# Kernel tuning notes

Measured on AMD Instinct MI355X. Metric: run time of the kernel, lower is better.

## Reference

```python
import jax, jax.numpy as jnp
import numpy as np

EPS = 1e-5

def layernorm(x, gamma, beta):
    mu = jnp.mean(x, axis=-1, keepdims=True)
    var = jnp.var(x, axis=-1, keepdims=True)
    return (x - mu) * jax.lax.rsqrt(var + EPS) * gamma + beta

def setup_inputs() -> dict:
    key = jax.random.key(0)
    ks = jax.random.split(key, 8)
    B, N, D, H, Dh, M = 2, 2048, 768, 12, 64, 3072
    s = 0.02
    return {
        "x": jax.random.normal(ks[0], (B, N, D), jnp.float32),
        "Wqkv": jax.random.normal(ks[1], (D, 3 * H * Dh), jnp.float32) * s,
        "Wout": jax.random.normal(ks[2], (H * Dh, D), jnp.float32) * s,
        "gamma1": jnp.ones((D,), jnp.float32),
        "beta1": jnp.zeros((D,), jnp.float32),
        "gamma2": jnp.ones((D,), jnp.float32),
        "beta2": jnp.zeros((D,), jnp.float32),
        "W1": jax.random.normal(ks[3], (D, M), jnp.float32) * s,
        "b1": jnp.zeros((M,), jnp.float32),
        "W2": jax.random.normal(ks[4], (M, D), jnp.float32) * s,
        "b2": jnp.zeros((D,), jnp.float32),
        "attn_bias": jax.random.normal(ks[5], (1, H, N, N), jnp.float32) * 0.1,
    }

def reference(x, Wqkv, Wout, gamma1, beta1, gamma2, beta2, W1, b1, W2, b2, attn_bias):
    B, N, D = x.shape
    H = attn_bias.shape[1]
    Dh = Wqkv.shape[1] // (3 * H)
    scale = Dh ** -0.5
    # Attention block (pre-norm)
    h = layernorm(x, gamma1, beta1)
    qkv = h @ Wqkv                              # [B, N, 3*H*Dh]
    qkv = qkv.reshape(B, N, 3, H, Dh)
    q, k, v = (jnp.transpose(qkv[:, :, i], (0, 2, 1, 3)) for i in range(3))  # [B, H, N, Dh]
    dots = jnp.einsum('bhqd,bhkd->bhqk', q, k) * scale
    # pos_info == 'mul_att_normed'
    attn = jax.nn.softmax(dots, axis=-1) * jax.nn.softmax(attn_bias, axis=-1)
    attn = attn / jnp.sum(attn, axis=-1, keepdims=True)
    out = jnp.einsum('bhqk,bhkd->bhqd', attn, v)          # [B, H, N, Dh]
    out = jnp.transpose(out, (0, 2, 1, 3)).reshape(B, N, H * Dh)
    x = out @ Wout + x
    # FeedForward block (pre-norm)
    h = layernorm(x, gamma2, beta2)
    h = jax.nn.gelu(h @ W1 + b1, approximate=False)
    x = h @ W2 + b2 + x
    return x
```

## Files before the change

### kernel.cpp

```cpp
#include <hip/hip_runtime.h>

typedef unsigned short u16t;
typedef __bf16 bf16x8 __attribute__((ext_vector_type(8)));
typedef float  f32x4  __attribute__((ext_vector_type(4)));
typedef float  f32x16 __attribute__((ext_vector_type(16)));
typedef unsigned u32x2 __attribute__((ext_vector_type(2)));
typedef unsigned u32x4 __attribute__((ext_vector_type(4)));

#define DEV __device__ __forceinline__

DEV u16t f32_to_bf16(float f) {
    unsigned u = __float_as_uint(f);
    unsigned r = (u + 0x7FFFu + ((u >> 16) & 1u)) >> 16;
    return (u16t)r;
}
DEV float bf16_to_f32(u16t u) { return __uint_as_float((unsigned)u << 16); }

DEV unsigned cvt_pk_bf16(float lo, float hi) {
    unsigned r;
    asm("v_cvt_pk_bf16_f32 %0, %1, %2" : "=v"(r) : "v"(lo), "v"(hi));
    return r;
}

DEV float gelu_exact(float x) {
    return 0.5f * x * (1.0f + erff(x * 0.70710678118654752f));
}

DEV void glds16(const void* g, void* l) {
    __builtin_amdgcn_global_load_lds(
        (const __attribute__((address_space(1))) void*)g,
        (__attribute__((address_space(3))) void*)l, 16, 0, 0);
}

#define SCHED_FENCE() __builtin_amdgcn_sched_barrier(0)

#define WAITN_BARRIER(N)                                          \
    asm volatile("s_waitcnt vmcnt(" #N ")" ::: "memory");         \
    SCHED_FENCE();                                                \
    __builtin_amdgcn_s_barrier();                                 \
    SCHED_FENCE();

#define PLAIN_BARRIER()                                           \
    SCHED_FENCE();                                                \
    __builtin_amdgcn_s_barrier();                                 \
    SCHED_FENCE();

__global__ __launch_bounds__(192)
void ln_kernel(const float* __restrict__ x, const float* __restrict__ g,
               const float* __restrict__ b, u16t* __restrict__ out)
{
    const int row = blockIdx.x;
    const int t = threadIdx.x;
    const f32x4 v = *reinterpret_cast<const f32x4*>(x + (size_t)row * 768 + t * 4);
    float s  = v[0] + v[1] + v[2] + v[3];
    float s2 = v[0] * v[0] + v[1] * v[1] + v[2] * v[2] + v[3] * v[3];
#pragma unroll
    for (int off = 32; off > 0; off >>= 1) {
        s  += __shfl_xor(s, off);
        s2 += __shfl_xor(s2, off);
    }
    __shared__ float sm[6];
    const int w = t >> 6;
    if ((t & 63) == 0) { sm[w] = s; sm[3 + w] = s2; }
    __syncthreads();
    s  = sm[0] + sm[1] + sm[2];
    s2 = sm[3] + sm[4] + sm[5];
    const float mu  = s * (1.0f / 768.0f);
    const float var = fmaxf(s2 * (1.0f / 768.0f) - mu * mu, 0.0f);
    const float rst = rsqrtf(var + 1e-5f);
    const f32x4 gv = *reinterpret_cast<const f32x4*>(g + t * 4);
    const f32x4 bv = *reinterpret_cast<const f32x4*>(b + t * 4);
    u32x2 r;
    r[0] = cvt_pk_bf16((v[0] - mu) * rst * gv[0] + bv[0],
                       (v[1] - mu) * rst * gv[1] + bv[1]);
    r[1] = cvt_pk_bf16((v[2] - mu) * rst * gv[2] + bv[2],
                       (v[3] - mu) * rst * gv[3] + bv[3]);
    *reinterpret_cast<u32x2*>(out + (size_t)row * 768 + t * 4) = r;
}

__global__ __launch_bounds__(256)
void transpose_all(const float* __restrict__ Wqkv, const float* __restrict__ Wout,
                   const float* __restrict__ W1, const float* __restrict__ W2,
                   u16t* __restrict__ WqkvT, u16t* __restrict__ WoutT,
                   u16t* __restrict__ W1T, u16t* __restrict__ W2T)
{
    int b = blockIdx.x;
    const float* in; u16t* out; int R, C, cx, ry;
    if (b < 432)       { in = Wqkv; out = WqkvT; R = 768;  C = 2304; cx = b % 36; ry = b / 36; }
    else if (b < 576)  { b -= 432;  in = Wout; out = WoutT; R = 768;  C = 768;  cx = b % 12; ry = b / 12; }
    else if (b < 1152) { b -= 576;  in = W1;   out = W1T;   R = 768;  C = 3072; cx = b % 48; ry = b / 48; }
    else               { b -= 1152; in = W2;   out = W2T;   R = 3072; C = 768;  cx = b % 12; ry = b / 12; }
    __shared__ float tile[64][65];
    const int c0 = cx * 64, r0 = ry * 64;
    const int t = threadIdx.x;
#pragma unroll
    for (int j = 0; j < 16; ++j) {
        const int idx = j * 256 + t;
        const int rl = idx >> 6, cl = idx & 63;
        tile[rl][cl] = in[(size_t)(r0 + rl) * C + c0 + cl];
    }
    __syncthreads();
#pragma unroll
    for (int j = 0; j < 16; ++j) {
        const int idx = j * 256 + t;
        const int cl = idx >> 6, rl = idx & 63;
        out[(size_t)(c0 + cl) * R + r0 + rl] = f32_to_bf16(tile[rl][cl]);
    }
}

template <int MODE, int TM>
__global__ __launch_bounds__(256)
void gemm_kernel(const u16t* __restrict__ A, const u16t* __restrict__ BT,
                 float* __restrict__ Cf, u16t* __restrict__ Cb,
                 const float* __restrict__ bias, const float* __restrict__ res,
                 u16t* __restrict__ Qo, u16t* __restrict__ Ko,
                 u16t* __restrict__ VTo,
                 int M, int Nn, int K)
{
    constexpr int MI = TM / 32;
    constexpr int ABYTES = TM * 128;
    __shared__ __align__(16) char gsm[ABYTES + 16384];
    const int t = threadIdx.x;
    const int w = t >> 6, lane = t & 63;
    const int l16 = lane & 15, lhi = lane >> 4;
    const int wr = w >> 1, wc = w & 1;
    const int m0 = blockIdx.x * TM, n0 = blockIdx.y * 128;

    const f32x4 fz = {0.f, 0.f, 0.f, 0.f};
    f32x4 acc[MI][4];
#pragma unroll
    for (int i = 0; i < MI; ++i)
#pragma unroll
        for (int j = 0; j < 4; ++j) acc[i][j] = fz;

    const int rbase = t >> 3;
    const int ssrc = ((t & 7) ^ (rbase & 7)) * 16;

    auto stage = [&](int kt) {
#pragma unroll
        for (int i = 0; i < TM / 32; ++i) {
            const int row = i * 32 + rbase;
            glds16((const char*)A + ((size_t)(m0 + row) * K + kt) * 2 + ssrc,
                   gsm + i * 4096 + t * 16);
        }
#pragma unroll
        for (int i = 0; i < 4; ++i) {
            const int row = i * 32 + rbase;
            glds16((const char*)BT + ((size_t)(n0 + row) * K + kt) * 2 + ssrc,
                   gsm + ABYTES + i * 4096 + t * 16);
        }
    };

    auto body = [&]() {
        const char* Ab = gsm;
        const char* Bb = gsm + ABYTES;
#pragma unroll
        for (int ks = 0; ks < 2; ++ks) {
            const int wsl = lhi + 4 * ks;
            bf16x8 af[MI], bfv[4];
#pragma unroll
            for (int i = 0; i < MI; ++i) {
                const int row = 16 * MI * wr + 16 * i + l16;
                af[i] = *reinterpret_cast<const bf16x8*>(
                    Ab + row * 128 + ((wsl ^ (row & 7)) << 4));
            }
#pragma unroll
            for (int j = 0; j < 4; ++j) {
                const int row = 64 * wc + 16 * j + l16;
                bfv[j] = *reinterpret_cast<const bf16x8*>(
                    Bb + row * 128 + ((wsl ^ (row & 7)) << 4));
            }
#pragma unroll
            for (int i = 0; i < MI; ++i)
#pragma unroll
                for (int j = 0; j < 4; ++j)
                    acc[i][j] = __builtin_amdgcn_mfma_f32_16x16x32_bf16(
                        af[i], bfv[j], acc[i][j], 0, 0, 0);
        }
    };

    for (int kt = 0; kt < K; kt += 64) {
        stage(kt);
        __syncthreads();
        body();
        __syncthreads();
    }

    const int rb = m0 + 16 * MI * wr + 4 * lhi;
    const int cb = n0 + 64 * wc + l16;

    if constexpr (MODE == 3) {
        const int qi = n0 / 768;
        const int b = rb >> 11;
        const int nn0 = rb & 2047;
#pragma unroll
        for (int j = 0; j < 4; ++j) {
            const int c = cb - qi * 768 + 16 * j;
            const int h = c >> 6, d = c & 63;
            if (qi < 2) {
                u16t* dst = (qi == 0) ? Qo : Ko;
                const size_t base = ((size_t)(b * 12 + h) * 2048 + nn0) * 64 + d;
#pragma unroll
                for (int i = 0; i < MI; ++i)
#pragma unroll
                    for (int r = 0; r < 4; ++r)
                        dst[base + (size_t)(16 * i + r) * 64] =
                            f32_to_bf16(acc[i][j][r]);
            } else {
                u16t* dst = VTo + ((size_t)(b * 12 + h) * 64 + d) * 2048 + nn0;
#pragma unroll
                for (int i = 0; i < MI; ++i) {
                    u32x2 pr;
                    pr[0] = cvt_pk_bf16(acc[i][j][0], acc[i][j][1]);
                    pr[1] = cvt_pk_bf16(acc[i][j][2], acc[i][j][3]);
                    *reinterpret_cast<u32x2*>(dst + 16 * i) = pr;
                }
            }
        }
        return;
    }

#pragma unroll
    for (int i = 0; i < MI; ++i) {
#pragma unroll
        for (int j = 0; j < 4; ++j) {
#pragma unroll
            for (int r = 0; r < 4; ++r) {
                const int row = rb + 16 * i + r;
                const int col = cb + 16 * j;
                float v = acc[i][j][r];
                if (MODE == 0) {
                    Cf[(size_t)row * Nn + col] = v;
                } else if (MODE == 1) {
                    v += res[(size_t)row * Nn + col];
                    if (bias) v += bias[col];
                    Cf[(size_t)row * Nn + col] = v;
                } else if (MODE == 2) {
                    v = gelu_exact(v + bias[col]);
                    Cb[(size_t)row * Nn + col] = f32_to_bf16(v);
                }
            }
        }
    }
}

__global__ __launch_bounds__(256, 2)
void attn_kernel(const u16t* __restrict__ Q, const u16t* __restrict__ K,
                 const u16t* __restrict__ VT, const float* __restrict__ bias,
                 u16t* __restrict__ Opart, float* __restrict__ Lpart)
{
    const int SEQ = 2048;
    const int h = blockIdx.y;
    const int ks = blockIdx.z;
    const int t = threadIdx.x;
    const int w = t >> 6, lane = t & 63;
    const int l32 = lane & 31, hi = lane >> 5;
    const int q = blockIdx.x * 128 + w * 32 + l32;
    const int bh0 = h, bh1 = 12 + h;

    __shared__ __align__(16) char smem[65536];

    const u16t* qp0 = Q + ((size_t)bh0 * SEQ + q) * 64 + 8 * hi;
    const u16t* qp1 = Q + ((size_t)bh1 * SEQ + q) * 64 + 8 * hi;
    bf16x8 qf0[4], qf1[4];
#pragma unroll
    for (int dseg = 0; dseg < 4; ++dseg) {
        qf0[dseg] = *reinterpret_cast<const bf16x8*>(qp0 + dseg * 16);
        qf1[dseg] = *reinterpret_cast<const bf16x8*>(qp1 + dseg * 16);
    }

    const char* kg0 = (const char*)K + (size_t)bh0 * SEQ * 128;
    const char* kg1 = (const char*)K + (size_t)bh1 * SEQ * 128;
    const char* vg0 = (const char*)VT + (size_t)bh0 * 64 * 4096;
    const char* vg1 = (const char*)VT + (size_t)bh1 * 64 * 4096;
    const char* bg = (const char*)bias +
                     ((size_t)h * SEQ + blockIdx.x * 128) * 8192;

    const int srow8 = lane >> 3;
    const int sslotK = ((lane & 7) ^ srow8) * 16;
    const int vrow  = w * 16 + (lane >> 2);
    const int sslotV = ((lane & 3) ^ ((vrow >> 1) & 3)) * 16;

    auto stage_all = [&](int bb, int k0) {
#pragma unroll
        for (int i = 0; i < 4; ++i) {
            const int row = 32 * w + 8 * i + srow8;
            glds16(bg + (size_t)row * 8192 + (size_t)k0 * 4 + sslotK,
                   smem + bb + 4096 * w + i * 1024);
        }
        glds16(kg0 + (size_t)(k0 + 8 * w + srow8) * 128 + sslotK,
               smem + bb + 16384 + w * 1024);
        glds16(kg1 + (size_t)(k0 + 8 * w + srow8) * 128 + sslotK,
               smem + bb + 20480 + w * 1024);
        glds16(vg0 + (size_t)vrow * 4096 + (size_t)k0 * 2 + sslotV,
               smem + bb + 24576 + w * 1024);
        glds16(vg1 + (size_t)vrow * 4096 + (size_t)k0 * 2 + sslotV,
               smem + bb + 28672 + w * 1024);
    };

    const int rsw = l32 & 7;
    int boff[4], koff[4];
#pragma unroll
    for (int g = 0; g < 4; ++g)
        boff[g] = (32 * w + l32) * 128 + ((((g << 1) + hi) ^ rsw) << 4);
#pragma unroll
    for (int dseg = 0; dseg < 4; ++dseg)
        koff[dseg] = l32 * 128 + ((((dseg << 1) + hi) ^ rsw) << 4);
    const int vr3 = (l32 >> 1) & 3;
    const int voff00 = l32 * 64 + ((hi ^ vr3) << 4);
    const int voff01 = l32 * 64 + (((2 + hi) ^ vr3) << 4);
    const int voff10 = voff00 + 32 * 64;
    const int voff11 = voff01 + 32 * 64;

    f32x16 o00, o01, o10, o11;
#pragma unroll
    for (int i = 0; i < 16; ++i) { o00[i] = 0.f; o01[i] = 0.f;
                                   o10[i] = 0.f; o11[i] = 0.f; }
    float lsum0 = 0.f, lsum1 = 0.f;

    auto batch_body = [&](const bf16x8 (&qf)[4], int kvbase, int vbase,
                          const f32x4 (&bv)[4], f32x16& oa, f32x16& ob,
                          float& lsum) {
        f32x16 st;
#pragma unroll
        for (int i = 0; i < 16; ++i) st[i] = 0.f;
#pragma unroll
        for (int dseg = 0; dseg < 4; ++dseg) {
            bf16x8 kf = *reinterpret_cast<const bf16x8*>(
                smem + kvbase + koff[dseg]);
            st = __builtin_amdgcn_mfma_f32_32x32x16_bf16(kf, qf[dseg], st, 0, 0, 0);
        }
        unsigned pk[8];
#pragma unroll
        for (int i2 = 0; i2 < 8; ++i2) {
            const int ia = 2 * i2, ib = 2 * i2 + 1;
            const float pa = __expf(st[ia] * 0.125f + bv[ia >> 2][ia & 3]);
            const float pb = __expf(st[ib] * 0.125f + bv[ib >> 2][ib & 3]);
            lsum += pa + pb;
            pk[i2] = cvt_pk_bf16(pa, pb);
        }
        unsigned sx[8];
#pragma unroll
        for (int i2 = 0; i2 < 8; ++i2)
            sx[i2] = (unsigned)__shfl_xor((int)pk[i2], 32);
        union { unsigned u[4]; bf16x8 v; } B0, B1;
        B0.u[0] = hi ? sx[2] : pk[0];
        B0.u[1] = hi ? sx[3] : pk[1];
        B0.u[2] = hi ? pk[2] : sx[0];
        B0.u[3] = hi ? pk[3] : sx[1];
        B1.u[0] = hi ? sx[6] : pk[4];
        B1.u[1] = hi ? sx[7] : pk[5];
        B1.u[2] = hi ? pk[6] : sx[4];
        B1.u[3] = hi ? pk[7] : sx[5];
        bf16x8 v00 = *reinterpret_cast<const bf16x8*>(smem + vbase + voff00);
        bf16x8 v01 = *reinterpret_cast<const bf16x8*>(smem + vbase + voff01);
        bf16x8 v10 = *reinterpret_cast<const bf16x8*>(smem + vbase + voff10);
        bf16x8 v11 = *reinterpret_cast<const bf16x8*>(smem + vbase + voff11);
        oa = __builtin_amdgcn_mfma_f32_32x32x16_bf16(v00, B0.v, oa, 0, 0, 0);
        oa = __builtin_amdgcn_mfma_f32_32x32x16_bf16(v01, B1.v, oa, 0, 0, 0);
        ob = __builtin_amdgcn_mfma_f32_32x32x16_bf16(v10, B0.v, ob, 0, 0, 0);
        ob = __builtin_amdgcn_mfma_f32_32x32x16_bf16(v11, B1.v, ob, 0, 0, 0);
    };

    const int kbeg = ks * 512;

    stage_all(0, kbeg);
    WAITN_BARRIER(0)

    int cur = 0;
    for (int i = 0; i < 16; ++i) {
        const int k0 = kbeg + 32 * i;
        if (i < 15) {
            stage_all(cur ^ 32768, k0 + 32);
            WAITN_BARRIER(8)
        } else {
            WAITN_BARRIER(0)
        }
        {
            f32x4 bv[4];
#pragma unroll
            for (int g = 0; g < 4; ++g)
                bv[g] = *reinterpret_cast<const f32x4*>(smem + cur + boff[g]);
            batch_body(qf0, cur + 16384, cur + 24576, bv, o00, o01, lsum0);
            batch_body(qf1, cur + 20480, cur + 28672, bv, o10, o11, lsum1);
        }
        PLAIN_BARRIER()
        cur ^= 32768;
    }

    lsum0 += __shfl_xor(lsum0, 32);
    lsum1 += __shfl_xor(lsum1, 32);

#pragma unroll
    for (int beta = 0; beta < 2; ++beta) {
        const int bh = beta ? bh1 : bh0;
        const f32x16& oa = beta ? o10 : o00;
        const f32x16& ob = beta ? o11 : o01;
        const float ls = beta ? lsum1 : lsum0;
        u16t* op = Opart + ((size_t)(ks * 24 + bh) * SEQ + q) * 64;
#pragma unroll
        for (int dh = 0; dh < 2; ++dh) {
            const f32x16& o = dh ? ob : oa;
#pragma unroll
            for (int g = 0; g < 4; ++g) {
                u32x2 pr;
                pr[0] = cvt_pk_bf16(o[4 * g], o[4 * g + 1]);
                pr[1] = cvt_pk_bf16(o[4 * g + 2], o[4 * g + 3]);
                *reinterpret_cast<u32x2*>(op + dh * 32 + 8 * g + 4 * hi) = pr;
            }
        }
        if (!hi)
            Lpart[(size_t)(ks * 24 + bh) * SEQ + q] = ls;
    }
}

__global__ __launch_bounds__(256)
void attn_combine(const u16t* __restrict__ Opart,
                  const float* __restrict__ Lpart, u16t* __restrict__ out)
{
    const int idx = blockIdx.x * 256 + threadIdx.x;
    const int dg = idx & 7;
    const int q = (idx >> 3) & 2047;
    const int bh = idx >> 14;
    const int b = bh / 12, h = bh % 12;
    const size_t base = ((size_t)bh * 2048 + q) * 64 + dg * 8;
    const size_t stride = (size_t)24 * 2048 * 64;
    float acc[8] = {0.f, 0.f, 0.f, 0.f, 0.f, 0.f, 0.f, 0.f};
    float l = 0.f;
#pragma unroll
    for (int j = 0; j < 4; ++j) {
        const u32x4 a = *reinterpret_cast<const u32x4*>(Opart + base + j * stride);
#pragma unroll
        for (int m = 0; m < 4; ++m) {
            acc[2 * m]     += bf16_to_f32((u16t)(a[m] & 0xFFFF));
            acc[2 * m + 1] += bf16_to_f32((u16t)(a[m] >> 16));
        }
        l += Lpart[(size_t)j * 24 * 2048 + bh * 2048 + q];
    }
    const float inv = 1.0f / l;
    u32x4 r;
#pragma unroll
    for (int m = 0; m < 4; ++m)
        r[m] = cvt_pk_bf16(acc[2 * m] * inv, acc[2 * m + 1] * inv);
    *reinterpret_cast<u32x4*>(
        out + ((size_t)(b * 2048 + q)) * 768 + h * 64 + dg * 8) = r;
}

extern "C" void kernel_launch(void* const* d_in, const int* in_sizes, int n_in,
                              void* d_out, int out_size, void* d_ws, size_t ws_size,
                              hipStream_t stream)
{
    const float* x    = (const float*)d_in[0];
    const float* Wqkv = (const float*)d_in[1];
    const float* Wout = (const float*)d_in[2];
    const float* g1   = (const float*)d_in[3];
    const float* be1  = (const float*)d_in[4];
    const float* g2   = (const float*)d_in[5];
    const float* be2  = (const float*)d_in[6];
    const float* W1   = (const float*)d_in[7];
    const float* b1   = (const float*)d_in[8];
    const float* W2   = (const float*)d_in[9];
    const float* b2   = (const float*)d_in[10];
    const float* ab   = (const float*)d_in[11];
    float* outp = (float*)d_out;

    char* ws = (char*)d_ws;
    size_t off = 0;
    auto alloc = [&](size_t bytes) -> char* {
        char* p = ws + off;
        off += (bytes + 255) & ~(size_t)255;
        return p;
    };

    u16t* WqkvT = (u16t*)alloc((size_t)2304 * 768 * 2);
    u16t* WoutT = (u16t*)alloc((size_t)768 * 768 * 2);
    u16t* W1T   = (u16t*)alloc((size_t)3072 * 768 * 2);
    u16t* W2T   = (u16t*)alloc((size_t)768 * 3072 * 2);
    u16t* h1    = (u16t*)alloc((size_t)4096 * 768 * 2);
    u16t* Qb    = (u16t*)alloc((size_t)24 * 2048 * 64 * 2);
    u16t* Kb    = (u16t*)alloc((size_t)24 * 2048 * 64 * 2);
    u16t* VTb   = (u16t*)alloc((size_t)24 * 64 * 2048 * 2);
    u16t* attnb = (u16t*)alloc((size_t)4096 * 768 * 2);
    float* x1   = (float*)alloc((size_t)4096 * 768 * 4);
    u16t* h2    = (u16t*)alloc((size_t)4096 * 768 * 2);
    u16t* Opart = (u16t*)alloc((size_t)4 * 24 * 2048 * 64 * 2);
    float* Lpart = (float*)alloc((size_t)4 * 24 * 2048 * 4);
    u16t* act   = (u16t*)alloc((size_t)4096 * 3072 * 2);

    transpose_all<<<1728, 256, 0, stream>>>(Wqkv, Wout, W1, W2,
                                            WqkvT, WoutT, W1T, W2T);

    ln_kernel<<<4096, 192, 0, stream>>>(x, g1, be1, h1);
    gemm_kernel<3, 128><<<dim3(32, 18), 256, 0, stream>>>(
        h1, WqkvT, nullptr, nullptr, nullptr, nullptr, Qb, Kb, VTb,
        4096, 2304, 768);
    attn_kernel<<<dim3(16, 12, 4), 256, 0, stream>>>(Qb, Kb, VTb, ab, Opart, Lpart);
    attn_combine<<<(24 * 2048 * 8) / 256, 256, 0, stream>>>(Opart, Lpart, attnb);
    gemm_kernel<1, 64><<<dim3(64, 6), 256, 0, stream>>>(
        attnb, WoutT, x1, nullptr, nullptr, x, nullptr, nullptr, nullptr,
        4096, 768, 768);

    ln_kernel<<<4096, 192, 0, stream>>>(x1, g2, be2, h2);
    gemm_kernel<2, 128><<<dim3(32, 24), 256, 0, stream>>>(
        h2, W1T, nullptr, act, b1, nullptr, nullptr, nullptr, nullptr,
        4096, 3072, 768);
    gemm_kernel<1, 64><<<dim3(64, 6), 256, 0, stream>>>(
        act, W2T, outp, nullptr, b2, x1, nullptr, nullptr, nullptr,
        4096, 768, 3072);
}
```

Measured before the change: 221.9 us.

## Double-buffer LDS in output GEMMs and store residual stream in bf16

Adds an optional double-buffered LDS pipeline to the GEMM kernel so the next K-tile's global-to-LDS loads overlap the current tile's MFMA work. It is enabled for the two 64-row-tile output projections, including the K=3072 FFN down-projection. Separately, the intermediate residual x1 is now stored in bf16 rather than fp32, which halves its write and its two reads (second layernorm and final residual add). The bf16 residual loses precision in the skip connection, and the doubled LDS footprint may lower occupancy.

```diff
diff --git a/kernel.cpp b/kernel.cpp
--- a/kernel.cpp
+++ b/kernel.cpp
@@ -45,13 +45,25 @@
     __builtin_amdgcn_s_barrier();                                 \
     SCHED_FENCE();
 
+template <bool INBF>
 __global__ __launch_bounds__(192)
-void ln_kernel(const float* __restrict__ x, const float* __restrict__ g,
+void ln_kernel(const void* __restrict__ xin, const float* __restrict__ g,
                const float* __restrict__ b, u16t* __restrict__ out)
 {
     const int row = blockIdx.x;
     const int t = threadIdx.x;
-    const f32x4 v = *reinterpret_cast<const f32x4*>(x + (size_t)row * 768 + t * 4);
+    f32x4 v;
+    if constexpr (INBF) {
+        const u32x2 ld = *reinterpret_cast<const u32x2*>(
+            (const u16t*)xin + (size_t)row * 768 + t * 4);
+        v[0] = bf16_to_f32((u16t)(ld[0] & 0xFFFF));
+        v[1] = bf16_to_f32((u16t)(ld[0] >> 16));
+        v[2] = bf16_to_f32((u16t)(ld[1] & 0xFFFF));
+        v[3] = bf16_to_f32((u16t)(ld[1] >> 16));
+    } else {
+        v = *reinterpret_cast<const f32x4*>(
+            (const float*)xin + (size_t)row * 768 + t * 4);
+    }
     float s  = v[0] + v[1] + v[2] + v[3];
     float s2 = v[0] * v[0] + v[1] * v[1] + v[2] * v[2] + v[3] * v[3];
 #pragma unroll
@@ -108,18 +120,20 @@
     }
 }
 
-template <int MODE, int TM>
+template <int MODE, int TM, bool DBUF, bool OUTBF, bool RESBF>
 __global__ __launch_bounds__(256)
 void gemm_kernel(const u16t* __restrict__ A, const u16t* __restrict__ BT,
                  float* __restrict__ Cf, u16t* __restrict__ Cb,
                  const float* __restrict__ bias, const float* __restrict__ res,
+                 const u16t* __restrict__ resb,
                  u16t* __restrict__ Qo, u16t* __restrict__ Ko,
                  u16t* __restrict__ VTo,
                  int M, int Nn, int K)
 {
     constexpr int MI = TM / 32;
     constexpr int ABYTES = TM * 128;
-    __shared__ __align__(16) char gsm[ABYTES + 16384];
+    constexpr int BUFB = ABYTES + 16384;
+    __shared__ __align__(16) char gsm[(DBUF ? 2 : 1) * BUFB];
     const int t = threadIdx.x;
     const int w = t >> 6, lane = t & 63;
     const int l16 = lane & 15, lhi = lane >> 4;
@@ -136,24 +150,24 @@
     const int rbase = t >> 3;
     const int ssrc = ((t & 7) ^ (rbase & 7)) * 16;
 
-    auto stage = [&](int kt) {
+    auto stage = [&](int bufb, int kt) {
 #pragma unroll
         for (int i = 0; i < TM / 32; ++i) {
             const int row = i * 32 + rbase;
             glds16((const char*)A + ((size_t)(m0 + row) * K + kt) * 2 + ssrc,
-                   gsm + i * 4096 + t * 16);
+                   gsm + bufb + i * 4096 + t * 16);
         }
 #pragma unroll
         for (int i = 0; i < 4; ++i) {
             const int row = i * 32 + rbase;
             glds16((const char*)BT + ((size_t)(n0 + row) * K + kt) * 2 + ssrc,
-                   gsm + ABYTES + i * 4096 + t * 16);
+                   gsm + bufb + ABYTES + i * 4096 + t * 16);
         }
     };
 
-    auto body = [&]() {
-        const char* Ab = gsm;
-        const char* Bb = gsm + ABYTES;
+    auto body = [&](int bufb) {
+        const char* Ab = gsm + bufb;
+        const char* Bb = gsm + bufb + ABYTES;
 #pragma unroll
         for (int ks = 0; ks < 2; ++ks) {
             const int wsl = lhi + 4 * ks;
@@ -179,11 +193,26 @@
         }
     };
 
-    for (int kt = 0; kt < K; kt += 64) {
-        stage(kt);
-        __syncthreads();
-        body();
-        __syncthreads();
+    if constexpr (DBUF) {
+        stage(0, 0);
+        int bufb = 0;
+        for (int kt = 0; kt + 64 < K; kt += 64) {
+            stage(bufb ^ BUFB, kt + 64);
+            if constexpr (TM == 128) { WAITN_BARRIER(8) }
+            else                     { WAITN_BARRIER(6) }
+            body(bufb);
+            PLAIN_BARRIER()
+            bufb ^= BUFB;
+        }
+        WAITN_BARRIER(0)
+        body(bufb);
+    } else {
+        for (int kt = 0; kt < K; kt += 64) {
+            stage(0, kt);
+            __syncthreads();
+            body(0);
+            __syncthreads();
+        }
     }
 
     const int rb = m0 + 16 * MI * wr + 4 * lhi;
@@ -228,16 +257,19 @@
             for (int r = 0; r < 4; ++r) {
                 const int row = rb + 16 * i + r;
                 const int col = cb + 16 * j;
+                const size_t idx = (size_t)row * Nn + col;
                 float v = acc[i][j][r];
-                if (MODE == 0) {
-                    Cf[(size_t)row * Nn + col] = v;
-                } else if (MODE == 1) {
-                    v += res[(size_t)row * Nn + col];
+                if constexpr (MODE == 0) {
+                    Cf[idx] = v;
+                } else if constexpr (MODE == 1) {
+                    if constexpr (RESBF) v += bf16_to_f32(resb[idx]);
+                    else                 v += res[idx];
                     if (bias) v += bias[col];
-                    Cf[(size_t)row * Nn + col] = v;
-                } else if (MODE == 2) {
+                    if constexpr (OUTBF) Cb[idx] = f32_to_bf16(v);
+                    else                 Cf[idx] = v;
+                } else if constexpr (MODE == 2) {
                     v = gelu_exact(v + bias[col]);
-                    Cb[(size_t)row * Nn + col] = f32_to_bf16(v);
+                    Cb[idx] = f32_to_bf16(v);
                 }
             }
         }
@@ -481,7 +513,7 @@
     u16t* Kb    = (u16t*)alloc((size_t)24 * 2048 * 64 * 2);
     u16t* VTb   = (u16t*)alloc((size_t)24 * 64 * 2048 * 2);
     u16t* attnb = (u16t*)alloc((size_t)4096 * 768 * 2);
-    float* x1   = (float*)alloc((size_t)4096 * 768 * 4);
+    u16t* x1b   = (u16t*)alloc((size_t)4096 * 768 * 2);
     u16t* h2    = (u16t*)alloc((size_t)4096 * 768 * 2);
     u16t* Opart = (u16t*)alloc((size_t)4 * 24 * 2048 * 64 * 2);
     float* Lpart = (float*)alloc((size_t)4 * 24 * 2048 * 4);
@@ -490,21 +522,21 @@
     transpose_all<<<1728, 256, 0, stream>>>(Wqkv, Wout, W1, W2,
                                             WqkvT, WoutT, W1T, W2T);
 
-    ln_kernel<<<4096, 192, 0, stream>>>(x, g1, be1, h1);
-    gemm_kernel<3, 128><<<dim3(32, 18), 256, 0, stream>>>(
-        h1, WqkvT, nullptr, nullptr, nullptr, nullptr, Qb, Kb, VTb,
+    ln_kernel<false><<<4096, 192, 0, stream>>>(x, g1, be1, h1);
+    gemm_kernel<3, 128, false, false, false><<<dim3(32, 18), 256, 0, stream>>>(
+        h1, WqkvT, nullptr, nullptr, nullptr, nullptr, nullptr, Qb, Kb, VTb,
         4096, 2304, 768);
     attn_kernel<<<dim3(16, 12, 4), 256, 0, stream>>>(Qb, Kb, VTb, ab, Opart, Lpart);
     attn_combine<<<(24 * 2048 * 8) / 256, 256, 0, stream>>>(Opart, Lpart, attnb);
-    gemm_kernel<1, 64><<<dim3(64, 6), 256, 0, stream>>>(
-        attnb, WoutT, x1, nullptr, nullptr, x, nullptr, nullptr, nullptr,
+    gemm_kernel<1, 64, true, true, false><<<dim3(64, 6), 256, 0, stream>>>(
+        attnb, WoutT, nullptr, x1b, nullptr, x, nullptr, nullptr, nullptr, nullptr,
         4096, 768, 768);
 
-    ln_kernel<<<4096, 192, 0, stream>>>(x1, g2, be2, h2);
-    gemm_kernel<2, 128><<<dim3(32, 24), 256, 0, stream>>>(
-        h2, W1T, nullptr, act, b1, nullptr, nullptr, nullptr, nullptr,
+    ln_kernel<true><<<4096, 192, 0, stream>>>(x1b, g2, be2, h2);
+    gemm_kernel<2, 128, false, false, false><<<dim3(32, 24), 256, 0, stream>>>(
+        h2, W1T, nullptr, act, b1, nullptr, nullptr, nullptr, nullptr, nullptr,
         4096, 3072, 768);
-    gemm_kernel<1, 64><<<dim3(64, 6), 256, 0, stream>>>(
-        act, W2T, outp, nullptr, b2, x1, nullptr, nullptr, nullptr,
+    gemm_kernel<1, 64, true, false, true><<<dim3(64, 6), 256, 0, stream>>>(
+        act, W2T, outp, nullptr, b2, nullptr, x1b, nullptr, nullptr, nullptr,
         4096, 768, 3072);
 }
```

Result: faster. 208.5 us, median of 2 (-6.1%).
